# Optimization experiments

Hardware: AMD Instinct MI355X
Metric: run time of the kernel (lower is better)

## Reference

```python
import jax, jax.numpy as jnp
import numpy as np

N = 100000
IN_C = 128
HID = 16
HEADS = 8
OUT_C = 64
E = 1600000
NEG_SLOPE = 0.2
EPS = 1e-16


def setup_inputs() -> dict:
    key = jax.random.key(0)
    ks = jax.random.split(key, 12)
    s = lambda k, shape, fan: jax.random.normal(k, shape, jnp.float32) * (1.0 / np.sqrt(fan))
    return {
        "x": jax.random.normal(ks[0], (N, IN_C), jnp.float32),
        "edge_index": jax.random.randint(ks[1], (2, E), 0, N, jnp.int64),
        # conv1 params (heads=8, concat=True)
        "W1": s(ks[2], (IN_C, HEADS * HID), IN_C),
        "a_src1": s(ks[3], (HEADS, HID), HID),
        "a_dst1": s(ks[4], (HEADS, HID), HID),
        "b1": jnp.zeros((HEADS * HID,), jnp.float32),
        # conv2 params (heads=1, concat=False)
        "W2": s(ks[5], (HEADS * HID, OUT_C), HEADS * HID),
        "a_src2": s(ks[6], (1, OUT_C), OUT_C),
        "a_dst2": s(ks[7], (1, OUT_C), OUT_C),
        "b2": jnp.zeros((OUT_C,), jnp.float32),
    }


def gat_conv(x, src, dst, W, a_src, a_dst, bias, concat):
    """PyG-style GATConv: edge softmax over incoming edges + scatter-add."""
    H, C = a_src.shape
    n = x.shape[0]
    h = (x @ W).reshape(n, H, C)                      # [N,H,C]
    asrc = jnp.einsum("nhc,hc->nh", h, a_src)          # [N,H]
    adst = jnp.einsum("nhc,hc->nh", h, a_dst)          # [N,H]
    e = jax.nn.leaky_relu(asrc[src] + adst[dst], NEG_SLOPE)  # [E,H]
    # numerically-stable segment softmax over edges sharing a destination
    m = jax.ops.segment_max(e, dst, num_segments=n)    # [N,H]
    m = jnp.where(jnp.isfinite(m), m, 0.0)
    ex = jnp.exp(e - m[dst])                           # [E,H]
    denom = jax.ops.segment_sum(ex, dst, num_segments=n)  # [N,H]
    alpha = ex / (denom[dst] + EPS)                    # [E,H]
    out = jax.ops.segment_sum(alpha[:, :, None] * h[src], dst, num_segments=n)  # [N,H,C]
    out = out.reshape(n, H * C) if concat else out.mean(axis=1)
    return out + bias


def reference(x, edge_index, W1, a_src1, a_dst1, b1, W2, a_src2, a_dst2, b2):
    n = x.shape[0]
    # PyG GATConv adds self-loops by default
    loop = jnp.arange(n, dtype=edge_index.dtype)
    src = jnp.concatenate([edge_index[0], loop])
    dst = jnp.concatenate([edge_index[1], loop])
    # dropout(p=0.6) is identity at inference
    h = jax.nn.elu(gat_conv(x, src, dst, W1, a_src1, a_dst1, b1, concat=True))
    return gat_conv(h, src, dst, W2, a_src2, a_dst2, b2, concat=False)
```

## Files before the change

### kernel.cpp

```cpp
#include <hip/hip_runtime.h>
#include <hip/hip_bf16.h>
#include <math.h>


typedef __attribute__((ext_vector_type(8))) short short8;
typedef __attribute__((ext_vector_type(4))) float f32x4;

__device__ __forceinline__ float bflo(uint u) { return __uint_as_float(u << 16); }
__device__ __forceinline__ float bfhi(uint u) { return __uint_as_float(u & 0xffff0000u); }
__device__ __forceinline__ float bf1(ushort v) { return __uint_as_float(((uint)v) << 16); }
__device__ __forceinline__ ushort f2bf(float f) {
    uint u = __float_as_uint(f);
    u += 0x7fff + ((u >> 16) & 1);
    return (ushort)(u >> 16);
}
#define LOG2E 1.44269504088896f

#define CSR_CAP 4096

__global__ __launch_bounds__(256) void k_bhist(const int* __restrict__ dst, int e,
                                               int* __restrict__ bcount) {
    __shared__ int h[1024];
    int t = threadIdx.x;
    for (int i = t; i < 1024; i += 256) h[i] = 0;
    __syncthreads();
    int c0 = blockIdx.x * 4096, c1 = min(c0 + 4096, e);
    for (int i = c0 + t; i < c1; i += 256) atomicAdd(&h[dst[i] >> 7], 1);
    __syncthreads();
    for (int i = t; i < 1024; i += 256)
        if (h[i]) atomicAdd(&bcount[i], h[i]);
}

__global__ __launch_bounds__(256) void k_bscan(const int* __restrict__ bcount, int nb, int n,
                                               int* __restrict__ ebase, int* __restrict__ ecur,
                                               int* __restrict__ cbase) {
    __shared__ int ae[1024], be[1024], ac[1024], bc[1024];
    int t = threadIdx.x;
    for (int i = t; i < 1024; i += 256) {
        int v = 0, nn = 0;
        if (i < nb) {
            v = bcount[i];
            nn = min(128, n - (i << 7));
        }
        ae[i] = v;
        ac[i] = v + nn;
    }
    __syncthreads();
    int* pa = ae; int* qa = be; int* pc = ac; int* qc = bc;
    for (int off = 1; off < 1024; off <<= 1) {
        for (int i = t; i < 1024; i += 256) {
            int va = pa[i], vc = pc[i];
            if (i >= off) { va += pa[i - off]; vc += pc[i - off]; }
            qa[i] = va; qc[i] = vc;
        }
        __syncthreads();
        int* tm = pa; pa = qa; qa = tm;
        tm = pc; pc = qc; qc = tm;
    }
    for (int i = t; i < 1024; i += 256) {
        if (i < nb) {
            int ea = (i == 0) ? 0 : pa[i - 1];
            int ca = (i == 0) ? 0 : pc[i - 1];
            ebase[i] = ea; ecur[i] = ea; cbase[i] = ca;
        }
    }
}

__global__ __launch_bounds__(512) void k_part(const int* __restrict__ src,
                                              const int* __restrict__ dst, int e,
                                              int* __restrict__ ecur, int* __restrict__ ebuf) {
    __shared__ int h[1024];
    __shared__ int base[1024];
    int t = threadIdx.x;
    int c0 = blockIdx.x * 8192, c1 = min(c0 + 8192, e);
    for (int i = t; i < 1024; i += 512) h[i] = 0;
    __syncthreads();
    for (int i = c0 + t; i < c1; i += 512) atomicAdd(&h[dst[i] >> 7], 1);
    __syncthreads();
    for (int i = t; i < 1024; i += 512) {
        int c = h[i];
        base[i] = c ? atomicAdd(&ecur[i], c) : 0;
        h[i] = 0;
    }
    __syncthreads();
    for (int i = c0 + t; i < c1; i += 512) {
        int d = dst[i], b = d >> 7;
        int r = atomicAdd(&h[b], 1);
        ebuf[base[b] + r] = (src[i] << 7) | (d & 127);
    }
}

__global__ __launch_bounds__(256) void k_build(const int* __restrict__ ebuf,
                                               const int* __restrict__ bcount,
                                               const int* __restrict__ ebase,
                                               const int* __restrict__ cbase,
                                               int* __restrict__ rowptr,
                                               int* __restrict__ csr,
                                               int* __restrict__ dstid, int n, int nb) {
    __shared__ int cnt[128];
    __shared__ int sc[128], sc2[128];
    __shared__ int csr_l[CSR_CAP];
    __shared__ int dst_l[CSR_CAP];
    int b = blockIdx.x, t = threadIdx.x;
    int n0 = b << 7;
    int nn = min(128, n - n0);
    int ec = bcount[b], eb = ebase[b], cb = cbase[b];
    if (t < 128) cnt[t] = 0;
    __syncthreads();
    for (int i = t; i < ec; i += 256) atomicAdd(&cnt[ebuf[eb + i] & 127], 1);
    __syncthreads();
    if (t < 128) sc[t] = (t < nn) ? cnt[t] + 1 : 0;
    __syncthreads();
    int* p = sc; int* q = sc2;
    for (int off = 1; off < 128; off <<= 1) {
        if (t < 128) {
            int v = p[t];
            if (t >= off) v += p[t - off];
            q[t] = v;
        }
        __syncthreads();
        int* tm = p; p = q; q = tm;
    }
    int total = p[127];
    if (total <= CSR_CAP) {
        if (t < nn) {
            int off = (t == 0) ? 0 : p[t - 1];
            rowptr[n0 + t] = cb + off;
            csr_l[off] = n0 + t;
            dst_l[off] = n0 + t;
            cnt[t] = off + 1;
        }
        __syncthreads();
        for (int i = t; i < ec; i += 256) {
            int v = ebuf[eb + i];
            int d = v & 127;
            int s = atomicAdd(&cnt[d], 1);
            csr_l[s] = v >> 7;
            dst_l[s] = n0 + d;
        }
        __syncthreads();
        for (int i = t; i < total; i += 256) {
            csr[cb + i] = csr_l[i];
            dstid[cb + i] = dst_l[i];
        }
    } else {
        if (t < nn) {
            int off = (t == 0) ? 0 : p[t - 1];
            rowptr[n0 + t] = cb + off;
            csr[cb + off] = n0 + t;
            dstid[cb + off] = n0 + t;
            cnt[t] = off + 1;
        }
        __syncthreads();
        for (int i = t; i < ec; i += 256) {
            int v = ebuf[eb + i];
            int d = v & 127;
            int s = atomicAdd(&cnt[d], 1);
            csr[cb + s] = v >> 7;
            dstid[cb + s] = n0 + d;
        }
    }
    if (b == nb - 1 && t == 0) rowptr[n] = cb + total;
}

template <int COLS, bool XBF16>
__global__ __launch_bounds__(256) void k_gemm_mfma(const void* __restrict__ Xv,
                                                   const float* __restrict__ W,
                                                   ushort* __restrict__ Y, int n) {
    __shared__ ushort As[128][136];
    __shared__ ushort Ws[COLS][136];
    const int t = threadIdx.x;
    const int row0 = blockIdx.x * 128;
    if constexpr (!XBF16) {
        const float* X = (const float*)Xv;
#pragma unroll
        for (int q = 0; q < 16; q++) {
            int idx = t + q * 256;
            int r = idx >> 5, c4 = (idx & 31) * 4;
            float4 xv = make_float4(0.f, 0.f, 0.f, 0.f);
            if (row0 + r < n) xv = *reinterpret_cast<const float4*>(&X[(size_t)(row0 + r) * 128 + c4]);
            ushort4 w4 = make_ushort4(f2bf(xv.x), f2bf(xv.y), f2bf(xv.z), f2bf(xv.w));
            *reinterpret_cast<ushort4*>(&As[r][c4]) = w4;
        }
    } else {
        const ushort* X = (const ushort*)Xv;
#pragma unroll
        for (int q = 0; q < 8; q++) {
            int idx = t + q * 256;
            int r = idx >> 4, c8 = (idx & 15) * 8;
            uint4 v = make_uint4(0u, 0u, 0u, 0u);
            if (row0 + r < n) v = *reinterpret_cast<const uint4*>(&X[(size_t)(row0 + r) * 128 + c8]);
            *reinterpret_cast<uint4*>(&As[r][c8]) = v;
        }
    }
    for (int i = t; i < 128 * COLS; i += 256) {
        int k = i / COLS, nc = i % COLS;
        Ws[nc][k] = f2bf(W[i]);
    }
    __syncthreads();
    const int w = t >> 6, l = t & 63;
    const int lr = l & 15;
    const int lk = (l >> 4) * 8;
    f32x4 acc[2][COLS / 16];
#pragma unroll
    for (int m = 0; m < 2; m++)
#pragma unroll
        for (int nb = 0; nb < COLS / 16; nb++) acc[m][nb] = (f32x4){0.f, 0.f, 0.f, 0.f};
#pragma unroll
    for (int kc = 0; kc < 128; kc += 32) {
        short8 a0 = *reinterpret_cast<const short8*>(&As[w * 32 + lr][kc + lk]);
        short8 a1 = *reinterpret_cast<const short8*>(&As[w * 32 + 16 + lr][kc + lk]);
#pragma unroll
        for (int nb = 0; nb < COLS / 16; nb++) {
            short8 bf = *reinterpret_cast<const short8*>(&Ws[nb * 16 + lr][kc + lk]);
            acc[0][nb] = __builtin_amdgcn_mfma_f32_16x16x32_bf16(a0, bf, acc[0][nb], 0, 0, 0);
            acc[1][nb] = __builtin_amdgcn_mfma_f32_16x16x32_bf16(a1, bf, acc[1][nb], 0, 0, 0);
        }
    }
#pragma unroll
    for (int m = 0; m < 2; m++)
#pragma unroll
        for (int j = 0; j < 4; j++) {
            int r = row0 + w * 32 + m * 16 + (l >> 4) * 4 + j;
            if (r < n) {
#pragma unroll
                for (int nb = 0; nb < COLS / 16; nb++)
                    Y[(size_t)r * COLS + nb * 16 + lr] = f2bf(acc[m][nb][j]);
            }
        }
}

__global__ void k_attn1(const uint* __restrict__ hu, const float* __restrict__ a_src,
                        const float* __restrict__ a_dst, float* __restrict__ asrc,
                        float* __restrict__ adst, int n) {
    int t = blockIdx.x * 256 + threadIdx.x;
    if (t >= n * 8) return;
    int node = t >> 3, hd = t & 7;
    const uint* hp = hu + (size_t)node * 64 + hd * 8;
    float s1 = 0.f, s2 = 0.f;
#pragma unroll
    for (int q = 0; q < 8; q++) {
        uint u = hp[q];
        float v0 = bflo(u), v1 = bfhi(u);
        s1 = fmaf(v0, a_src[hd * 16 + 2 * q], s1);
        s1 = fmaf(v1, a_src[hd * 16 + 2 * q + 1], s1);
        s2 = fmaf(v0, a_dst[hd * 16 + 2 * q], s2);
        s2 = fmaf(v1, a_dst[hd * 16 + 2 * q + 1], s2);
    }
    asrc[t] = s1 * LOG2E;
    adst[t] = s2 * LOG2E;
}
__global__ void k_attn2(const uint* __restrict__ hu, const float* __restrict__ a_src,
                        const float* __restrict__ a_dst, float* __restrict__ asrc,
                        float* __restrict__ adst, int n) {
    int t = blockIdx.x * 256 + threadIdx.x;
    if (t >= n * 8) return;
    int node = t >> 3, j = t & 7;
    const uint* hp = hu + (size_t)node * 32 + j * 4;
    float s1 = 0.f, s2 = 0.f;
#pragma unroll
    for (int q = 0; q < 4; q++) {
        uint u = hp[q];
        float v0 = bflo(u), v1 = bfhi(u);
        s1 = fmaf(v0, a_src[j * 8 + 2 * q], s1);
        s1 = fmaf(v1, a_src[j * 8 + 2 * q + 1], s1);
        s2 = fmaf(v0, a_dst[j * 8 + 2 * q], s2);
        s2 = fmaf(v1, a_dst[j * 8 + 2 * q + 1], s2);
    }
#pragma unroll
    for (int o = 1; o < 8; o <<= 1) {
        s1 += __shfl_xor(s1, o);
        s2 += __shfl_xor(s2, o);
    }
    if (j == 0) { asrc[node] = s1 * LOG2E; adst[node] = s2 * LOG2E; }
}

__global__ void k_score1(const int* __restrict__ csr, const int* __restrict__ dstid,
                         const float* __restrict__ asrc, const float* __restrict__ adst,
                         _Float16* __restrict__ p1, int tot8) {
    int t = blockIdx.x * 256 + threadIdx.x;
    if (t >= tot8) return;
    int slot = t >> 3, hd = t & 7;
    int s = csr[slot], d = dstid[slot];
    float e = asrc[s * 8 + hd] + adst[d * 8 + hd];
    e = fmaxf(e, 0.2f * e);
    p1[t] = (_Float16)exp2f(e);
}
__global__ void k_score2(const int* __restrict__ csr, const int* __restrict__ dstid,
                         const float* __restrict__ asrc, const float* __restrict__ adst,
                         float* __restrict__ p2, int tot) {
    int t = blockIdx.x * 256 + threadIdx.x;
    if (t >= tot) return;
    float e = asrc[csr[t]] + adst[dstid[t]];
    e = fmaxf(e, 0.2f * e);
    p2[t] = exp2f(e);
}

__global__ __launch_bounds__(256) void k_agg1(
    const uint* __restrict__ hu, const _Float16* __restrict__ p1,
    const int* __restrict__ rowptr, const int* __restrict__ csr,
    const float* __restrict__ b1, uint* __restrict__ x2, int n) {
    int wid = (blockIdx.x * 256 + threadIdx.x) >> 6;
    if (wid >= n) return;
    uint lane = threadIdx.x & 63;
    uint c0 = lane * 2;
    uint hd = lane >> 3;
    int beg = rowptr[wid], end = rowptr[wid + 1];
    float s = 0.f, acc0 = 0.f, acc1 = 0.f;
    for (int base = beg; base < end; base += 64) {
        int cnt = min(64, end - base);
        int vidx = ((int)lane < cnt) ? csr[base + lane] : 0;
        const _Float16* pp = p1 + (size_t)base * 8 + hd;
        int j = 0;
        for (; j + 8 <= cnt; j += 8) {
            uint s0 = __builtin_amdgcn_readlane(vidx, j);
            uint s1 = __builtin_amdgcn_readlane(vidx, j + 1);
            uint s2 = __builtin_amdgcn_readlane(vidx, j + 2);
            uint s3 = __builtin_amdgcn_readlane(vidx, j + 3);
            uint s4 = __builtin_amdgcn_readlane(vidx, j + 4);
            uint s5 = __builtin_amdgcn_readlane(vidx, j + 5);
            uint s6 = __builtin_amdgcn_readlane(vidx, j + 6);
            uint s7 = __builtin_amdgcn_readlane(vidx, j + 7);
            uint u0 = hu[s0 * 64u + lane];
            uint u1 = hu[s1 * 64u + lane];
            uint u2 = hu[s2 * 64u + lane];
            uint u3 = hu[s3 * 64u + lane];
            uint u4 = hu[s4 * 64u + lane];
            uint u5 = hu[s5 * 64u + lane];
            uint u6 = hu[s6 * 64u + lane];
            uint u7 = hu[s7 * 64u + lane];
            float q0 = (float)pp[(j + 0) * 8];
            float q1 = (float)pp[(j + 1) * 8];
            float q2 = (float)pp[(j + 2) * 8];
            float q3 = (float)pp[(j + 3) * 8];
            float q4 = (float)pp[(j + 4) * 8];
            float q5 = (float)pp[(j + 5) * 8];
            float q6 = (float)pp[(j + 6) * 8];
            float q7 = (float)pp[(j + 7) * 8];
            s += ((q0 + q1) + (q2 + q3)) + ((q4 + q5) + (q6 + q7));
            acc0 = fmaf(q0, bflo(u0), fmaf(q1, bflo(u1), acc0));
            acc0 = fmaf(q2, bflo(u2), fmaf(q3, bflo(u3), acc0));
            acc0 = fmaf(q4, bflo(u4), fmaf(q5, bflo(u5), acc0));
            acc0 = fmaf(q6, bflo(u6), fmaf(q7, bflo(u7), acc0));
            acc1 = fmaf(q0, bfhi(u0), fmaf(q1, bfhi(u1), acc1));
            acc1 = fmaf(q2, bfhi(u2), fmaf(q3, bfhi(u3), acc1));
            acc1 = fmaf(q4, bfhi(u4), fmaf(q5, bfhi(u5), acc1));
            acc1 = fmaf(q6, bfhi(u6), fmaf(q7, bfhi(u7), acc1));
        }
        for (; j < cnt; ++j) {
            uint s0 = __builtin_amdgcn_readlane(vidx, j);
            float q0 = (float)pp[j * 8];
            uint u0 = hu[s0 * 64u + lane];
            s += q0;
            acc0 = fmaf(q0, bflo(u0), acc0);
            acc1 = fmaf(q0, bfhi(u0), acc1);
        }
    }
    float inv = 1.f / (s + 1e-16f);
    float o0 = acc0 * inv + b1[c0];
    float o1 = acc1 * inv + b1[c0 + 1];
    o0 = o0 > 0.f ? o0 : (__expf(o0) - 1.f);
    o1 = o1 > 0.f ? o1 : (__expf(o1) - 1.f);
    union { ushort b[2]; uint u; } pk;
    pk.b[0] = f2bf(o0);
    pk.b[1] = f2bf(o1);
    x2[(uint)wid * 64u + lane] = pk.u;
}
__global__ __launch_bounds__(256) void k_agg2(
    const ushort* __restrict__ hb, const float* __restrict__ p2,
    const int* __restrict__ rowptr, const int* __restrict__ csr,
    const float* __restrict__ b2, float* __restrict__ out, int n) {
    int wid = (blockIdx.x * 256 + threadIdx.x) >> 6;
    if (wid >= n) return;
    uint lane = threadIdx.x & 63;
    int beg = rowptr[wid], end = rowptr[wid + 1];
    float s = 0.f, acc = 0.f;
    for (int base = beg; base < end; base += 64) {
        int cnt = min(64, end - base);
        int vidx = ((int)lane < cnt) ? csr[base + lane] : 0;
        int pvi = ((int)lane < cnt) ? __float_as_int(p2[base + lane]) : 0;
        int j = 0;
        for (; j + 8 <= cnt; j += 8) {
            uint s0 = __builtin_amdgcn_readlane(vidx, j);
            uint s1 = __builtin_amdgcn_readlane(vidx, j + 1);
            uint s2 = __builtin_amdgcn_readlane(vidx, j + 2);
            uint s3 = __builtin_amdgcn_readlane(vidx, j + 3);
            uint s4 = __builtin_amdgcn_readlane(vidx, j + 4);
            uint s5 = __builtin_amdgcn_readlane(vidx, j + 5);
            uint s6 = __builtin_amdgcn_readlane(vidx, j + 6);
            uint s7 = __builtin_amdgcn_readlane(vidx, j + 7);
            float h0 = bf1(hb[s0 * 64u + lane]);
            float h1 = bf1(hb[s1 * 64u + lane]);
            float h2 = bf1(hb[s2 * 64u + lane]);
            float h3 = bf1(hb[s3 * 64u + lane]);
            float h4 = bf1(hb[s4 * 64u + lane]);
            float h5 = bf1(hb[s5 * 64u + lane]);
            float h6 = bf1(hb[s6 * 64u + lane]);
            float h7 = bf1(hb[s7 * 64u + lane]);
            float q0 = __int_as_float(__builtin_amdgcn_readlane(pvi, j));
            float q1 = __int_as_float(__builtin_amdgcn_readlane(pvi, j + 1));
            float q2 = __int_as_float(__builtin_amdgcn_readlane(pvi, j + 2));
            float q3 = __int_as_float(__builtin_amdgcn_readlane(pvi, j + 3));
            float q4 = __int_as_float(__builtin_amdgcn_readlane(pvi, j + 4));
            float q5 = __int_as_float(__builtin_amdgcn_readlane(pvi, j + 5));
            float q6 = __int_as_float(__builtin_amdgcn_readlane(pvi, j + 6));
            float q7 = __int_as_float(__builtin_amdgcn_readlane(pvi, j + 7));
            s += ((q0 + q1) + (q2 + q3)) + ((q4 + q5) + (q6 + q7));
            acc = fmaf(q0, h0, fmaf(q1, h1, acc));
            acc = fmaf(q2, h2, fmaf(q3, h3, acc));
            acc = fmaf(q4, h4, fmaf(q5, h5, acc));
            acc = fmaf(q6, h6, fmaf(q7, h7, acc));
        }
        for (; j < cnt; ++j) {
            uint s0 = __builtin_amdgcn_readlane(vidx, j);
            float q0 = __int_as_float(__builtin_amdgcn_readlane(pvi, j));
            float h0 = bf1(hb[s0 * 64u + lane]);
            s += q0;
            acc = fmaf(q0, h0, acc);
        }
    }
    out[(size_t)wid * 64 + lane] = acc / (s + 1e-16f) + b2[lane];
}

extern "C" void kernel_launch(void* const* d_in, const int* in_sizes, int n_in,
                              void* d_out, int out_size, void* d_ws, size_t ws_size,
                              hipStream_t stream) {
    const float* x   = (const float*)d_in[0];
    const int*   ei  = (const int*)d_in[1];
    const float* W1  = (const float*)d_in[2];
    const float* as1 = (const float*)d_in[3];
    const float* ad1 = (const float*)d_in[4];
    const float* b1  = (const float*)d_in[5];
    const float* W2  = (const float*)d_in[6];
    const float* as2 = (const float*)d_in[7];
    const float* ad2 = (const float*)d_in[8];
    const float* b2  = (const float*)d_in[9];
    float* out = (float*)d_out;

    int N = in_sizes[0] / 128;
    int E = in_sizes[1] / 2;
    int TOT = E + N;
    const int* src = ei;
    const int* dst = ei + E;

    char* p = (char*)d_ws;
    auto alloc = [&](size_t bytes) {
        char* r = p;
        p += (bytes + 255) & ~size_t(255);
        return r;
    };
    ushort* h1b  = (ushort*)alloc((size_t)N * 128 * 2);
    ushort* h2b  = (ushort*)alloc((size_t)N * 64 * 2);
    ushort* x2b  = (ushort*)alloc((size_t)N * 128 * 2);
    float* asrc1 = (float*)alloc((size_t)N * 8 * 4);
    float* adst1 = (float*)alloc((size_t)N * 8 * 4);
    float* asrc2 = (float*)alloc((size_t)N * 4);
    float* adst2 = (float*)alloc((size_t)N * 4);
    int* rowptr  = (int*)alloc((size_t)(N + 1) * 4);
    int* csr     = (int*)alloc((size_t)TOT * 4);
    int* dstid   = (int*)alloc((size_t)TOT * 4);
    int* ebuf    = (int*)alloc((size_t)TOT * 4);
    _Float16* p1 = (_Float16*)alloc(((size_t)TOT * 8 + 16) * 2);
    int* bcount  = (int*)alloc(1024 * 4);
    int* ebase   = (int*)alloc(1024 * 4);
    int* ecur    = (int*)alloc(1024 * 4);
    int* cbase   = (int*)alloc(1024 * 4);
    float* p2    = (float*)ebuf;

    int NB = (N + 127) >> 7;
    int nbk = (E + 4095) / 4096;
    int nbp = (E + 8191) / 8192;

    hipMemsetAsync(bcount, 0, 1024 * 4, stream);
    k_bhist<<<nbk, 256, 0, stream>>>(dst, E, bcount);
    k_bscan<<<1, 256, 0, stream>>>(bcount, NB, N, ebase, ecur, cbase);
    k_part<<<nbp, 512, 0, stream>>>(src, dst, E, ecur, ebuf);
    k_build<<<NB, 256, 0, stream>>>(ebuf, bcount, ebase, cbase, rowptr, csr, dstid, N, NB);

    int gb = (N + 127) / 128;
    k_gemm_mfma<128, false><<<gb, 256, 0, stream>>>(x, W1, h1b, N);
    k_attn1<<<(N * 8 + 255) / 256, 256, 0, stream>>>((const uint*)h1b, as1, ad1, asrc1, adst1, N);
    k_score1<<<((size_t)TOT * 8 + 255) / 256, 256, 0, stream>>>(csr, dstid, asrc1, adst1, p1, TOT * 8);
    k_agg1<<<(N + 3) / 4, 256, 0, stream>>>((const uint*)h1b, p1, rowptr, csr, b1, (uint*)x2b, N);

    k_gemm_mfma<64, true><<<gb, 256, 0, stream>>>(x2b, W2, h2b, N);
    k_attn2<<<(N * 8 + 255) / 256, 256, 0, stream>>>((const uint*)h2b, as2, ad2, asrc2, adst2, N);
    k_score2<<<(TOT + 255) / 256, 256, 0, stream>>>(csr, dstid, asrc2, adst2, p2, TOT);
    k_agg2<<<(N + 3) / 4, 256, 0, stream>>>((const ushort*)h2b, p2, rowptr, csr, b2, out, N);
}
```

Before: 269.9 us.

## Fuse edge score computation into aggregation kernels and drop dstid array

Removes the separate score kernels and computes leaky-relu/exp2 edge scores inside the per-destination aggregation wavefronts, staging them in shared memory. This eliminates the dstid array and the materialized p1/p2 score buffers, saving their global writes and reads. The histogram kernel also moves to larger blocks. In exchange, each aggregation wave does extra gathers of asrc and extra exp work inline, and relies on an LDS waitcnt without a barrier within a wave.

```diff
diff --git a/kernel.cpp b/kernel.cpp
--- a/kernel.cpp
+++ b/kernel.cpp
@@ -18,16 +18,16 @@
 
 #define CSR_CAP 4096
 
-__global__ __launch_bounds__(256) void k_bhist(const int* __restrict__ dst, int e,
+__global__ __launch_bounds__(512) void k_bhist(const int* __restrict__ dst, int e,
                                                int* __restrict__ bcount) {
     __shared__ int h[1024];
     int t = threadIdx.x;
-    for (int i = t; i < 1024; i += 256) h[i] = 0;
-    __syncthreads();
-    int c0 = blockIdx.x * 4096, c1 = min(c0 + 4096, e);
-    for (int i = c0 + t; i < c1; i += 256) atomicAdd(&h[dst[i] >> 7], 1);
-    __syncthreads();
-    for (int i = t; i < 1024; i += 256)
+    for (int i = t; i < 1024; i += 512) h[i] = 0;
+    __syncthreads();
+    int c0 = blockIdx.x * 8192, c1 = min(c0 + 8192, e);
+    for (int i = c0 + t; i < c1; i += 512) atomicAdd(&h[dst[i] >> 7], 1);
+    __syncthreads();
+    for (int i = t; i < 1024; i += 512)
         if (h[i]) atomicAdd(&bcount[i], h[i]);
 }
 
@@ -95,12 +95,10 @@
                                                const int* __restrict__ ebase,
                                                const int* __restrict__ cbase,
                                                int* __restrict__ rowptr,
-                                               int* __restrict__ csr,
-                                               int* __restrict__ dstid, int n, int nb) {
+                                               int* __restrict__ csr, int n, int nb) {
     __shared__ int cnt[128];
     __shared__ int sc[128], sc2[128];
     __shared__ int csr_l[CSR_CAP];
-    __shared__ int dst_l[CSR_CAP];
     int b = blockIdx.x, t = threadIdx.x;
     int n0 = b << 7;
     int nn = min(128, n - n0);
@@ -127,37 +125,28 @@
             int off = (t == 0) ? 0 : p[t - 1];
             rowptr[n0 + t] = cb + off;
             csr_l[off] = n0 + t;
-            dst_l[off] = n0 + t;
             cnt[t] = off + 1;
         }
         __syncthreads();
         for (int i = t; i < ec; i += 256) {
             int v = ebuf[eb + i];
-            int d = v & 127;
-            int s = atomicAdd(&cnt[d], 1);
+            int s = atomicAdd(&cnt[v & 127], 1);
             csr_l[s] = v >> 7;
-            dst_l[s] = n0 + d;
         }
         __syncthreads();
-        for (int i = t; i < total; i += 256) {
-            csr[cb + i] = csr_l[i];
-            dstid[cb + i] = dst_l[i];
-        }
+        for (int i = t; i < total; i += 256) csr[cb + i] = csr_l[i];
     } else {
         if (t < nn) {
             int off = (t == 0) ? 0 : p[t - 1];
             rowptr[n0 + t] = cb + off;
             csr[cb + off] = n0 + t;
-            dstid[cb + off] = n0 + t;
             cnt[t] = off + 1;
         }
         __syncthreads();
         for (int i = t; i < ec; i += 256) {
             int v = ebuf[eb + i];
-            int d = v & 127;
-            int s = atomicAdd(&cnt[d], 1);
+            int s = atomicAdd(&cnt[v & 127], 1);
             csr[cb + s] = v >> 7;
-            dstid[cb + s] = n0 + d;
         }
     }
     if (b == nb - 1 && t == 0) rowptr[n] = cb + total;
@@ -275,42 +264,34 @@
     if (j == 0) { asrc[node] = s1 * LOG2E; adst[node] = s2 * LOG2E; }
 }
 
-__global__ void k_score1(const int* __restrict__ csr, const int* __restrict__ dstid,
-                         const float* __restrict__ asrc, const float* __restrict__ adst,
-                         _Float16* __restrict__ p1, int tot8) {
-    int t = blockIdx.x * 256 + threadIdx.x;
-    if (t >= tot8) return;
-    int slot = t >> 3, hd = t & 7;
-    int s = csr[slot], d = dstid[slot];
-    float e = asrc[s * 8 + hd] + adst[d * 8 + hd];
-    e = fmaxf(e, 0.2f * e);
-    p1[t] = (_Float16)exp2f(e);
-}
-__global__ void k_score2(const int* __restrict__ csr, const int* __restrict__ dstid,
-                         const float* __restrict__ asrc, const float* __restrict__ adst,
-                         float* __restrict__ p2, int tot) {
-    int t = blockIdx.x * 256 + threadIdx.x;
-    if (t >= tot) return;
-    float e = asrc[csr[t]] + adst[dstid[t]];
-    e = fmaxf(e, 0.2f * e);
-    p2[t] = exp2f(e);
-}
-
 __global__ __launch_bounds__(256) void k_agg1(
-    const uint* __restrict__ hu, const _Float16* __restrict__ p1,
-    const int* __restrict__ rowptr, const int* __restrict__ csr,
-    const float* __restrict__ b1, uint* __restrict__ x2, int n) {
+    const uint* __restrict__ hu, const float* __restrict__ asrc,
+    const float* __restrict__ adst, const int* __restrict__ rowptr,
+    const int* __restrict__ csr, const float* __restrict__ b1,
+    uint* __restrict__ x2, int n) {
+    __shared__ float P[4][512];
+    int wv = threadIdx.x >> 6;
     int wid = (blockIdx.x * 256 + threadIdx.x) >> 6;
     if (wid >= n) return;
     uint lane = threadIdx.x & 63;
+    uint hd = lane >> 3;
+    uint sl = lane & 7;
     uint c0 = lane * 2;
-    uint hd = lane >> 3;
+    float adn = adst[(uint)wid * 8u + hd];
     int beg = rowptr[wid], end = rowptr[wid + 1];
     float s = 0.f, acc0 = 0.f, acc1 = 0.f;
     for (int base = beg; base < end; base += 64) {
         int cnt = min(64, end - base);
         int vidx = ((int)lane < cnt) ? csr[base + lane] : 0;
-        const _Float16* pp = p1 + (size_t)base * 8 + hd;
+#pragma unroll
+        for (int m = 0; m < 8; m++) {
+            int slot = 8 * m + (int)sl;
+            int cs = csr[base + min(slot, cnt - 1)];
+            float e = asrc[(uint)cs * 8u + hd] + adn;
+            e = fmaxf(e, 0.2f * e);
+            P[wv][slot * 8 + hd] = exp2f(e);
+        }
+        asm volatile("s_waitcnt lgkmcnt(0)" ::: "memory");
         int j = 0;
         for (; j + 8 <= cnt; j += 8) {
             uint s0 = __builtin_amdgcn_readlane(vidx, j);
@@ -329,14 +310,14 @@
             uint u5 = hu[s5 * 64u + lane];
             uint u6 = hu[s6 * 64u + lane];
             uint u7 = hu[s7 * 64u + lane];
-            float q0 = (float)pp[(j + 0) * 8];
-            float q1 = (float)pp[(j + 1) * 8];
-            float q2 = (float)pp[(j + 2) * 8];
-            float q3 = (float)pp[(j + 3) * 8];
-            float q4 = (float)pp[(j + 4) * 8];
-            float q5 = (float)pp[(j + 5) * 8];
-            float q6 = (float)pp[(j + 6) * 8];
-            float q7 = (float)pp[(j + 7) * 8];
+            float q0 = P[wv][(j + 0) * 8 + hd];
+            float q1 = P[wv][(j + 1) * 8 + hd];
+            float q2 = P[wv][(j + 2) * 8 + hd];
+            float q3 = P[wv][(j + 3) * 8 + hd];
+            float q4 = P[wv][(j + 4) * 8 + hd];
+            float q5 = P[wv][(j + 5) * 8 + hd];
+            float q6 = P[wv][(j + 6) * 8 + hd];
+            float q7 = P[wv][(j + 7) * 8 + hd];
             s += ((q0 + q1) + (q2 + q3)) + ((q4 + q5) + (q6 + q7));
             acc0 = fmaf(q0, bflo(u0), fmaf(q1, bflo(u1), acc0));
             acc0 = fmaf(q2, bflo(u2), fmaf(q3, bflo(u3), acc0));
@@ -349,7 +330,7 @@
         }
         for (; j < cnt; ++j) {
             uint s0 = __builtin_amdgcn_readlane(vidx, j);
-            float q0 = (float)pp[j * 8];
+            float q0 = P[wv][j * 8 + hd];
             uint u0 = hu[s0 * 64u + lane];
             s += q0;
             acc0 = fmaf(q0, bflo(u0), acc0);
@@ -367,18 +348,25 @@
     x2[(uint)wid * 64u + lane] = pk.u;
 }
 __global__ __launch_bounds__(256) void k_agg2(
-    const ushort* __restrict__ hb, const float* __restrict__ p2,
-    const int* __restrict__ rowptr, const int* __restrict__ csr,
-    const float* __restrict__ b2, float* __restrict__ out, int n) {
+    const ushort* __restrict__ hb, const float* __restrict__ asrc,
+    const float* __restrict__ adst, const int* __restrict__ rowptr,
+    const int* __restrict__ csr, const float* __restrict__ b2,
+    float* __restrict__ out, int n) {
+    __shared__ float P2[4][64];
+    int wv = threadIdx.x >> 6;
     int wid = (blockIdx.x * 256 + threadIdx.x) >> 6;
     if (wid >= n) return;
     uint lane = threadIdx.x & 63;
+    float adn = adst[wid];
     int beg = rowptr[wid], end = rowptr[wid + 1];
     float s = 0.f, acc = 0.f;
     for (int base = beg; base < end; base += 64) {
         int cnt = min(64, end - base);
-        int vidx = ((int)lane < cnt) ? csr[base + lane] : 0;
-        int pvi = ((int)lane < cnt) ? __float_as_int(p2[base + lane]) : 0;
+        int vidx = csr[base + min((int)lane, cnt - 1)];
+        float e = asrc[vidx] + adn;
+        e = fmaxf(e, 0.2f * e);
+        P2[wv][lane] = ((int)lane < cnt) ? exp2f(e) : 0.f;
+        asm volatile("s_waitcnt lgkmcnt(0)" ::: "memory");
         int j = 0;
         for (; j + 8 <= cnt; j += 8) {
             uint s0 = __builtin_amdgcn_readlane(vidx, j);
@@ -397,14 +385,14 @@
             float h5 = bf1(hb[s5 * 64u + lane]);
             float h6 = bf1(hb[s6 * 64u + lane]);
             float h7 = bf1(hb[s7 * 64u + lane]);
-            float q0 = __int_as_float(__builtin_amdgcn_readlane(pvi, j));
-            float q1 = __int_as_float(__builtin_amdgcn_readlane(pvi, j + 1));
-            float q2 = __int_as_float(__builtin_amdgcn_readlane(pvi, j + 2));
-            float q3 = __int_as_float(__builtin_amdgcn_readlane(pvi, j + 3));
-            float q4 = __int_as_float(__builtin_amdgcn_readlane(pvi, j + 4));
-            float q5 = __int_as_float(__builtin_amdgcn_readlane(pvi, j + 5));
-            float q6 = __int_as_float(__builtin_amdgcn_readlane(pvi, j + 6));
-            float q7 = __int_as_float(__builtin_amdgcn_readlane(pvi, j + 7));
+            float q0 = P2[wv][j + 0];
+            float q1 = P2[wv][j + 1];
+            float q2 = P2[wv][j + 2];
+            float q3 = P2[wv][j + 3];
+            float q4 = P2[wv][j + 4];
+            float q5 = P2[wv][j + 5];
+            float q6 = P2[wv][j + 6];
+            float q7 = P2[wv][j + 7];
             s += ((q0 + q1) + (q2 + q3)) + ((q4 + q5) + (q6 + q7));
             acc = fmaf(q0, h0, fmaf(q1, h1, acc));
             acc = fmaf(q2, h2, fmaf(q3, h3, acc));
@@ -413,7 +401,7 @@
         }
         for (; j < cnt; ++j) {
             uint s0 = __builtin_amdgcn_readlane(vidx, j);
-            float q0 = __int_as_float(__builtin_amdgcn_readlane(pvi, j));
+            float q0 = P2[wv][j];
             float h0 = bf1(hb[s0 * 64u + lane]);
             s += q0;
             acc = fmaf(q0, h0, acc);
@@ -458,33 +446,29 @@
     float* adst2 = (float*)alloc((size_t)N * 4);
     int* rowptr  = (int*)alloc((size_t)(N + 1) * 4);
     int* csr     = (int*)alloc((size_t)TOT * 4);
-    int* dstid   = (int*)alloc((size_t)TOT * 4);
-    int* ebuf    = (int*)alloc((size_t)TOT * 4);
-    _Float16* p1 = (_Float16*)alloc(((size_t)TOT * 8 + 16) * 2);
+    int* ebuf    = (int*)alloc((size_t)E * 4);
     int* bcount  = (int*)alloc(1024 * 4);
     int* ebase   = (int*)alloc(1024 * 4);
     int* ecur    = (int*)alloc(1024 * 4);
     int* cbase   = (int*)alloc(1024 * 4);
-    float* p2    = (float*)ebuf;
 
     int NB = (N + 127) >> 7;
-    int nbk = (E + 4095) / 4096;
     int nbp = (E + 8191) / 8192;
 
     hipMemsetAsync(bcount, 0, 1024 * 4, stream);
-    k_bhist<<<nbk, 256, 0, stream>>>(dst, E, bcount);
+    k_bhist<<<nbp, 512, 0, stream>>>(dst, E, bcount);
     k_bscan<<<1, 256, 0, stream>>>(bcount, NB, N, ebase, ecur, cbase);
     k_part<<<nbp, 512, 0, stream>>>(src, dst, E, ecur, ebuf);
-    k_build<<<NB, 256, 0, stream>>>(ebuf, bcount, ebase, cbase, rowptr, csr, dstid, N, NB);
+    k_build<<<NB, 256, 0, stream>>>(ebuf, bcount, ebase, cbase, rowptr, csr, N, NB);
 
     int gb = (N + 127) / 128;
     k_gemm_mfma<128, false><<<gb, 256, 0, stream>>>(x, W1, h1b, N);
     k_attn1<<<(N * 8 + 255) / 256, 256, 0, stream>>>((const uint*)h1b, as1, ad1, asrc1, adst1, N);
-    k_score1<<<((size_t)TOT * 8 + 255) / 256, 256, 0, stream>>>(csr, dstid, asrc1, adst1, p1, TOT * 8);
-    k_agg1<<<(N + 3) / 4, 256, 0, stream>>>((const uint*)h1b, p1, rowptr, csr, b1, (uint*)x2b, N);
+    k_agg1<<<(N + 3) / 4, 256, 0, stream>>>((const uint*)h1b, asrc1, adst1, rowptr, csr, b1,
+                                            (uint*)x2b, N);
 
     k_gemm_mfma<64, true><<<gb, 256, 0, stream>>>(x2b, W2, h2b, N);
     k_attn2<<<(N * 8 + 255) / 256, 256, 0, stream>>>((const uint*)h2b, as2, ad2, asrc2, adst2, N);
-    k_score2<<<(TOT + 255) / 256, 256, 0, stream>>>(csr, dstid, asrc2, adst2, p2, TOT);
-    k_agg2<<<(N + 3) / 4, 256, 0, stream>>>((const ushort*)h2b, p2, rowptr, csr, b2, out, N);
-}
+    k_agg2<<<(N + 3) / 4, 256, 0, stream>>>((const ushort*)h2b, asrc2, adst2, rowptr, csr, b2,
+                                            out, N);
+}
```

Measured after the change: 242.0 us. -10.3%, faster.
